# Kernel tuning notes

Hardware: AMD Instinct MI355X
Metric: run time of the kernel (lower is better)

## Reference

```python
import jax, jax.numpy as jnp
import numpy as np

D_MODEL = 1024
N_HEADS = 16
D_FF = 4096
EPS = 1e-6


def _linear_params(key, d_in, d_out):
    kw, kb = jax.random.split(key)
    bound = 1.0 / np.sqrt(d_in)
    W = jax.random.uniform(kw, (d_out, d_in), minval=-bound, maxval=bound, dtype=jnp.float32)
    b = jax.random.uniform(kb, (d_out,), minval=-bound, maxval=bound, dtype=jnp.float32)
    return W, b


def setup_inputs() -> dict:
    key = jax.random.key(0)
    keys = jax.random.split(key, 8)
    x = jax.random.normal(keys[0], (4, 2048, D_MODEL), dtype=jnp.float32)
    mask = jnp.ones((4, 1, 1, 2048), dtype=jnp.bool_)
    Wq, bq = _linear_params(keys[1], D_MODEL, D_MODEL)
    Wk, bk = _linear_params(keys[2], D_MODEL, D_MODEL)
    Wv, bv = _linear_params(keys[3], D_MODEL, D_MODEL)
    Wo, bo = _linear_params(keys[4], D_MODEL, D_MODEL)
    W1, b1 = _linear_params(keys[5], D_MODEL, D_FF)
    W2, b2 = _linear_params(keys[6], D_FF, D_MODEL)
    ln1_g = jnp.ones((D_MODEL,), jnp.float32); ln1_b = jnp.zeros((D_MODEL,), jnp.float32)
    ln2_g = jnp.ones((D_MODEL,), jnp.float32); ln2_b = jnp.zeros((D_MODEL,), jnp.float32)
    return {"x": x, "mask": mask,
            "Wq": Wq, "bq": bq, "Wk": Wk, "bk": bk, "Wv": Wv, "bv": bv,
            "Wo": Wo, "bo": bo, "W1": W1, "b1": b1, "W2": W2, "b2": b2,
            "ln1_g": ln1_g, "ln1_b": ln1_b, "ln2_g": ln2_g, "ln2_b": ln2_b}


def _layernorm(x, g, b):
    # torch LayerNorm here uses unbiased std and divides by (std + eps)
    mean = jnp.mean(x, axis=-1, keepdims=True)
    std = jnp.std(x, axis=-1, keepdims=True, ddof=1)
    return g * (x - mean) / (std + EPS) + b


def _gelu_tanh(x):
    c = np.sqrt(2.0 / np.pi).astype(np.float32)
    return 0.5 * x * (1.0 + jnp.tanh(c * (x + 0.044715 * x * x * x)))


def _mha(xn, mask, Wq, bq, Wk, bk, Wv, bv, Wo, bo):
    B, S, D = xn.shape
    d_k = D // N_HEADS
    def proj(W, b):
        y = jnp.einsum('bsd,ed->bse', xn, W) + b
        return y.reshape(B, S, N_HEADS, d_k).transpose(0, 2, 1, 3)  # [B,h,S,d_k]
    q, k, v = proj(Wq, bq), proj(Wk, bk), proj(Wv, bv)
    scores = jnp.einsum('bhqd,bhkd->bhqk', q, k) / np.float32(np.sqrt(d_k))
    scores = jnp.where(mask, scores, jnp.float32(-1e9))
    p = jax.nn.softmax(scores, axis=-1)
    o = jnp.einsum('bhqk,bhkd->bhqd', p, v)
    o = o.transpose(0, 2, 1, 3).reshape(B, S, D)
    return jnp.einsum('bsd,ed->bse', o, Wo) + bo


def reference(x, mask, Wq, bq, Wk, bk, Wv, bv, Wo, bo, W1, b1, W2, b2,
              ln1_g, ln1_b, ln2_g, ln2_b):
    xn = _layernorm(x, ln1_g, ln1_b)
    y = x + _mha(xn, mask, Wq, bq, Wk, bk, Wv, bv, Wo, bo)
    yn = _layernorm(y, ln2_g, ln2_b)
    h = _gelu_tanh(jnp.einsum('bsd,fd->bsf', yn, W1) + b1)
    z = y + (jnp.einsum('bsf,df->bsd', h, W2) + b2)
    return z
```

## Files before the change

### kernel.cpp

```cpp
#include <hip/hip_runtime.h>

typedef __bf16 bf16;
typedef __bf16 bfx4 __attribute__((ext_vector_type(4)));
typedef __bf16 bfx8 __attribute__((ext_vector_type(8)));
typedef float  fx4  __attribute__((ext_vector_type(4)));

#define NTOK 8192
#define DM   1024
#define DFF  4096
#define SEQ  2048
#define NH   16
#define DK   64

#define OFF_WQKV 0ull
#define OFF_WO   (OFF_WQKV + 3072ull*1024*2)
#define OFF_W1   (OFF_WO   + 1024ull*1024*2)
#define OFF_W2   (OFF_W1   + 4096ull*1024*2)
#define OFF_BQKV (OFF_W2   + 4096ull*1024*2)
#define OFF_XN   (OFF_BQKV + 3072ull*4)
#define OFF_QKV  (OFF_XN   + 8192ull*1024*2)
#define OFF_ATTN (OFF_QKV  + 8192ull*3072*2)
#define OFF_Y    (OFF_ATTN + 8192ull*1024*2)
#define OFF_VT   OFF_XN
#define OFF_H    OFF_XN
#define OFF_YN   OFF_ATTN

#define BARRIER() do { asm volatile("" ::: "memory"); \
                       __builtin_amdgcn_s_barrier();  \
                       asm volatile("" ::: "memory"); } while (0)

__device__ __forceinline__ void gload16(const void* g, void* l) {
  __builtin_amdgcn_global_load_lds(
      (__attribute__((address_space(1))) void*)(g),
      (__attribute__((address_space(3))) void*)(l), 16, 0, 0);
}

__device__ __forceinline__ float gelu_tanh(float x) {
  float u = 0.7978845608028654f * (x + 0.044715f * x * x * x);
  float t = 1.f - 2.f / (__expf(2.f * u) + 1.f);
  return 0.5f * x * (1.f + t);
}

__global__ __launch_bounds__(256) void castk(const float* __restrict__ s,
                                             bf16* __restrict__ d, int n) {
  int i = (blockIdx.x * 256 + threadIdx.x) * 4;
  if (i < n) {
    float4 v = *(const float4*)(s + i);
    bfx4 o;
    o[0] = (bf16)v.x; o[1] = (bf16)v.y; o[2] = (bf16)v.z; o[3] = (bf16)v.w;
    *(bfx4*)(d + i) = o;
  }
}

__global__ __launch_bounds__(256) void ln_kernel(const float* __restrict__ x,
                                                 const float* __restrict__ g,
                                                 const float* __restrict__ b,
                                                 bf16* __restrict__ out) {
  const int row = blockIdx.x;
  const int c = threadIdx.x * 4;
  const float4 v = *(const float4*)&x[(size_t)row * DM + c];
  float s1 = v.x + v.y + v.z + v.w;
  float s2 = v.x * v.x + v.y * v.y + v.z * v.z + v.w * v.w;
  #pragma unroll
  for (int o = 32; o; o >>= 1) { s1 += __shfl_xor(s1, o); s2 += __shfl_xor(s2, o); }
  __shared__ float red[8];
  const int wid = threadIdx.x >> 6;
  if ((threadIdx.x & 63) == 0) { red[wid] = s1; red[4 + wid] = s2; }
  __syncthreads();
  s1 = red[0] + red[1] + red[2] + red[3];
  s2 = red[4] + red[5] + red[6] + red[7];
  const float mean = s1 * (1.f / (float)DM);
  const float var = (s2 - (float)DM * mean * mean) * (1.f / (float)(DM - 1));
  const float inv = 1.f / (sqrtf(fmaxf(var, 0.f)) + 1e-6f);
  bfx4 o;
  o[0] = (bf16)(g[c + 0] * (v.x - mean) * inv + b[c + 0]);
  o[1] = (bf16)(g[c + 1] * (v.y - mean) * inv + b[c + 1]);
  o[2] = (bf16)(g[c + 2] * (v.z - mean) * inv + b[c + 2]);
  o[3] = (bf16)(g[c + 3] * (v.w - mean) * inv + b[c + 3]);
  *(bfx4*)&out[(size_t)row * DM + c] = o;
}

template <int NREP, int EPI>
__global__ __launch_bounds__(512, 2) void gemm256(const bf16* __restrict__ A,
                                                  const bf16* __restrict__ B,
                                                  const float* __restrict__ bias,
                                                  const float* __restrict__ resid,
                                                  void* __restrict__ outp,
                                                  int M, int N, int K) {
  extern __shared__ char lds[];
  constexpr int BHALF = NREP * 4096;
  const int tid = threadIdx.x;
  const int lane = tid & 63, w = tid >> 6;
  const int l15 = lane & 15, lhi = lane >> 4;
  const int wm = w >> 2, wn = w & 3;

  const int nwg = gridDim.x * gridDim.y;
  int bid = blockIdx.y * gridDim.x + blockIdx.x;
  bid = (bid & 7) * (nwg >> 3) + (bid >> 3);
  const int m0 = (bid % gridDim.x) * 256;
  const int n0 = (bid / gridDim.x) * (NREP * 64);

  const char* Ab = (const char*)A;
  const char* Bb = (const char*)B;
  const size_t str = (size_t)K * 2;

  const int r_s = tid >> 3;
  const int c2  = (tid & 7) * 16;
  const int csw = c2 ^ ((r_s & 7) << 4);

  auto stA = [&](int buf, int half, int kt) {
    const size_t kb = (size_t)kt * 128;
    #pragma unroll
    for (int s = 0; s < 2; ++s)
      gload16(Ab + (size_t)(m0 + half * 128 + s * 64 + r_s) * str + kb + csw,
              lds + (buf * 2 + half) * 16384 + s * 8192 + tid * 16);
  };
  auto stB = [&](int buf, int half, int kt) {
    const size_t kb = (size_t)kt * 128;
    #pragma unroll
    for (int s = 0; s < NREP / 2; ++s)
      gload16(Bb + (size_t)(n0 + half * (NREP * 32) + s * 64 + r_s) * str + kb + csw,
              lds + 65536 + (buf * 2 + half) * BHALF + s * 8192 + tid * 16);
  };

  fx4 acc[8][NREP] = {};
  bfx8 af[4][2];
  bfx8 bfv[NREP][2];
  const int asw = (l15 & 7) << 4;

  auto ldA = [&](int buf, int i0) {
    const char* base = lds + (buf * 2 + wm) * 16384;
    #pragma unroll
    for (int ii = 0; ii < 4; ++ii) {
      const int r = (i0 + ii) * 16 + l15;
      #pragma unroll
      for (int kk = 0; kk < 2; ++kk)
        af[ii][kk] = *(const bfx8*)(base + r * 128 + ((kk * 64 + lhi * 16) ^ asw));
    }
  };
  auto ldB = [&](int buf, int j0) {
    const char* base = lds + 65536 + (buf * 2 + (wn >> 1)) * BHALF;
    #pragma unroll
    for (int jj = 0; jj < NREP / 2; ++jj) {
      const int r = (wn & 1) * (NREP * 16) + (j0 + jj) * 16 + l15;
      #pragma unroll
      for (int kk = 0; kk < 2; ++kk)
        bfv[j0 + jj][kk] = *(const bfx8*)(base + r * 128 + ((kk * 64 + lhi * 16) ^ asw));
    }
  };
  auto mm = [&](int qm, int qn) {
    __builtin_amdgcn_s_setprio(1);
    #pragma unroll
    for (int ii = 0; ii < 4; ++ii)
      #pragma unroll
      for (int jj = 0; jj < NREP / 2; ++jj)
        #pragma unroll
        for (int kk = 0; kk < 2; ++kk)
          acc[qm * 4 + ii][qn * (NREP / 2) + jj] =
              __builtin_amdgcn_mfma_f32_16x16x32_bf16(
                  af[ii][kk], bfv[qn * (NREP / 2) + jj][kk],
                  acc[qm * 4 + ii][qn * (NREP / 2) + jj], 0, 0, 0);
    __builtin_amdgcn_s_setprio(0);
  };

  const int nK = K >> 6, niters = nK >> 1;

  stA(0, 0, 0); stA(0, 1, 0); stB(0, 0, 0); stB(0, 1, 0);
  stB(1, 0, 1); stB(1, 1, 1);
  asm volatile("s_waitcnt vmcnt(%0)" :: "i"(NREP) : "memory");
  BARRIER();

  #pragma unroll 1
  for (int it = 0; it < niters; ++it) {
    const int t1 = 2 * it + 1, t2 = 2 * it + 2, t3 = 2 * it + 3;
    const bool more = (it < niters - 1);
    ldA(0, 0); ldB(0, 0);
    stA(1, 0, t1);
    BARRIER(); mm(0, 0); BARRIER();
    ldB(0, NREP / 2);
    stA(1, 1, t1);
    BARRIER(); mm(0, 1); BARRIER();
    ldA(0, 4);
    if (more) stB(0, 0, t2);
    BARRIER(); mm(1, 0); BARRIER();
    if (more) {
      stB(0, 1, t2);
      asm volatile("s_waitcnt vmcnt(%0)" :: "i"(NREP) : "memory");
    } else {
      asm volatile("s_waitcnt vmcnt(0)" ::: "memory");
    }
    BARRIER(); mm(1, 1); BARRIER();
    ldA(1, 0); ldB(1, 0);
    if (more) stA(0, 0, t2);
    BARRIER(); mm(0, 0); BARRIER();
    ldB(1, NREP / 2);
    if (more) stA(0, 1, t2);
    BARRIER(); mm(0, 1); BARRIER();
    ldA(1, 4);
    if (more) stB(1, 0, t3);
    BARRIER(); mm(1, 0); BARRIER();
    if (more) {
      stB(1, 1, t3);
      asm volatile("s_waitcnt vmcnt(%0)" :: "i"(NREP) : "memory");
    }
    BARRIER(); mm(1, 1); BARRIER();
  }

  const int rb = m0 + wm * 128 + lhi * 4;
  const int cb = n0 + wn * 16 * NREP + l15;
  #pragma unroll
  for (int j = 0; j < NREP; ++j) {
    const int c = cb + j * 16;
    const float bv = bias[c];
    #pragma unroll
    for (int i = 0; i < 8; ++i) {
      #pragma unroll
      for (int e = 0; e < 4; ++e) {
        const size_t idx = (size_t)(rb + i * 16 + e) * N + c;
        float v = acc[i][j][e] + bv;
        if constexpr (EPI == 1) v = gelu_tanh(v);
        if constexpr (EPI == 2) {
          ((float*)outp)[idx] = v + resid[idx];
        } else {
          ((bf16*)outp)[idx] = (bf16)v;
        }
      }
    }
  }
}

__global__ __launch_bounds__(256) void vtrans(const bf16* __restrict__ QKV,
                                              bf16* __restrict__ VT) {
  __shared__ bf16 Ts[64][64];
  const int t = threadIdx.x;
  const int s0 = blockIdx.x * 64, bh = blockIdx.y;
  const int b = bh >> 4, h = bh & 15;
  const size_t tokb = (size_t)b * SEQ + s0;
  #pragma unroll
  for (int rr = 0; rr < 2; ++rr) {
    const int s = (t >> 3) + rr * 32;
    const int c0 = (t & 7) * 8;
    bfx8 v = *(const bfx8*)&QKV[(tokb + s) * 3072 + 2048 + h * 64 + c0];
    #pragma unroll
    for (int e = 0; e < 8; ++e) {
      const int d = c0 + e;
      Ts[d][(s + ((d >> 3) & 7) * 8) & 63] = v[e];
    }
  }
  __syncthreads();
  #pragma unroll
  for (int rr = 0; rr < 2; ++rr) {
    const int d = (t >> 3) + rr * 32;
    const int c0 = (t & 7) * 8;
    bfx8 v = *(const bfx8*)&Ts[d][(c0 + ((d >> 3) & 7) * 8) & 63];
    *(bfx8*)&VT[(size_t)(bh * 64 + d) * SEQ + s0 + c0] = v;
  }
}

__global__ __launch_bounds__(256) void attn_kernel(const bf16* __restrict__ QKV,
                                                   const bf16* __restrict__ VT,
                                                   bf16* __restrict__ O) {
  __shared__ bf16 lds[2][2][4096];
  const int tid = threadIdx.x;
  const int lane = tid & 63, w = tid >> 6;
  const int l15 = lane & 15, lhi = lane >> 4;
  int id = blockIdx.x;
  id = (id & 7) * 128 + (id >> 3);
  const int q0 = (id & 15) * 128;
  const int h = (id >> 4) & 15;
  const int b = id >> 8;
  const size_t tokbase = (size_t)b * SEQ;
  const char* Kb  = (const char*)QKV;
  const char* Vtb = (const char*)(VT + (size_t)((b * NH + h) * 64) * SEQ);

  fx4 acc[2][4] = {};
  float mrun[2] = {-3e38f, -3e38f};
  float lrun[2] = {0.f, 0.f};

  auto STAGE = [&](int t, int buf) {
    const int kv0 = t * 64;
    #pragma unroll
    for (int seg = 0; seg < 2; ++seg) {
      const int lin = (seg * 4 + w) * 1024 + lane * 16;
      const int row = lin >> 7, cbyte = lin & 127;
      const int cs = cbyte ^ ((row & 7) << 4);
      gload16(Kb + ((tokbase + kv0 + row) * 3072 + 1024 + h * 64) * 2 + cs,
              (char*)&lds[buf][0][0] + lin);
      gload16(Vtb + ((size_t)row * SEQ + kv0) * 2 + cs,
              (char*)&lds[buf][1][0] + lin);
    }
  };

  STAGE(0, 0);

  bfx8 qf[2][2];
  #pragma unroll
  for (int m = 0; m < 2; ++m)
    #pragma unroll
    for (int kk = 0; kk < 2; ++kk) {
      bfx8 raw = *(const bfx8*)&QKV[(tokbase + q0 + w * 32 + m * 16 + l15) * 3072
                                    + h * DK + kk * 32 + lhi * 8];
      bfx8 sc;
      #pragma unroll
      for (int e = 0; e < 8; ++e) sc[e] = (bf16)((float)raw[e] * 0.18033688011112042f);
      qf[m][kk] = sc;
    }

  const int NT = SEQ / 64;
  for (int t = 0; t < NT; ++t) {
    const int buf = t & 1;
    if (t + 1 < NT) {
      STAGE(t + 1, buf ^ 1);
      asm volatile("s_waitcnt vmcnt(4)" ::: "memory");
    } else {
      asm volatile("s_waitcnt vmcnt(0)" ::: "memory");
    }
    __builtin_amdgcn_s_barrier();

    const char* Kl = (const char*)&lds[buf][0][0];
    const char* Vl = (const char*)&lds[buf][1][0];

    fx4 s[2][4] = {};
    #pragma unroll
    for (int kk = 0; kk < 2; ++kk) {
      bfx8 kf[4];
      #pragma unroll
      for (int n = 0; n < 4; ++n) {
        const int row = n * 16 + l15;
        kf[n] = *(const bfx8*)(Kl + row * 128 + ((kk * 64 + lhi * 16) ^ ((row & 7) << 4)));
      }
      #pragma unroll
      for (int m = 0; m < 2; ++m)
        #pragma unroll
        for (int n = 0; n < 4; ++n)
          s[m][n] = __builtin_amdgcn_mfma_f32_16x16x32_bf16(kf[n], qf[m][kk], s[m][n], 0, 0, 0);
    }

    uint32_t pu[2][4][2];
    #pragma unroll
    for (int m = 0; m < 2; ++m) {
      float rm = s[m][0][0];
      #pragma unroll
      for (int n = 0; n < 4; ++n)
        #pragma unroll
        for (int e = 0; e < 4; ++e) rm = fmaxf(rm, s[m][n][e]);
      rm = fmaxf(rm, __shfl_xor(rm, 16));
      rm = fmaxf(rm, __shfl_xor(rm, 32));
      const float mnew = fmaxf(mrun[m], rm);
      const float alpha = exp2f(mrun[m] - mnew);
      mrun[m] = mnew;
      float rs = 0.f;
      #pragma unroll
      for (int n = 0; n < 4; ++n)
        #pragma unroll
        for (int e = 0; e < 4; ++e) {
          const float p = exp2f(s[m][n][e] - mnew);
          s[m][n][e] = p;
          rs += p;
        }
      rs += __shfl_xor(rs, 16);
      rs += __shfl_xor(rs, 32);
      lrun[m] = lrun[m] * alpha + rs;
      #pragma unroll
      for (int dn = 0; dn < 4; ++dn)
        #pragma unroll
        for (int e = 0; e < 4; ++e) acc[m][dn][e] *= alpha;
      #pragma unroll
      for (int n = 0; n < 4; ++n)
        #pragma unroll
        for (int p2 = 0; p2 < 2; ++p2) {
          union { bf16 h2[2]; uint32_t u; } cv;
          cv.h2[0] = (bf16)s[m][n][2 * p2];
          cv.h2[1] = (bf16)s[m][n][2 * p2 + 1];
          pu[m][n][p2] = cv.u;
        }
    }

    #pragma unroll
    for (int kk = 0; kk < 2; ++kk) {
      bfx8 pB[2];
      #pragma unroll
      for (int m = 0; m < 2; ++m) {
        union { uint32_t u[4]; bfx8 v; } cb2;
        cb2.u[0] = pu[m][2 * kk][0];
        cb2.u[1] = pu[m][2 * kk][1];
        cb2.u[2] = pu[m][2 * kk + 1][0];
        cb2.u[3] = pu[m][2 * kk + 1][1];
        pB[m] = cb2.v;
      }
      #pragma unroll
      for (int dn = 0; dn < 4; ++dn) {
        const int row = dn * 16 + l15;
        const int sw = (row & 7) << 4;
        union { bfx4 q2[2]; bfx8 v; } vv;
        vv.q2[0] = *(const bfx4*)(Vl + row * 128 + ((kk * 64 + lhi * 8) ^ sw));
        vv.q2[1] = *(const bfx4*)(Vl + row * 128 + ((kk * 64 + 32 + lhi * 8) ^ sw));
        #pragma unroll
        for (int m = 0; m < 2; ++m)
          acc[m][dn] = __builtin_amdgcn_mfma_f32_16x16x32_bf16(vv.v, pB[m], acc[m][dn], 0, 0, 0);
      }
    }

    asm volatile("s_waitcnt lgkmcnt(0)" ::: "memory");
    __builtin_amdgcn_s_barrier();
  }

  __syncthreads();
  bf16* Ep = &lds[0][0][0] + w * 2048;
  const float rinv0 = __builtin_amdgcn_rcpf(lrun[0]);
  const float rinv1 = __builtin_amdgcn_rcpf(lrun[1]);
  #pragma unroll
  for (int m = 0; m < 2; ++m) {
    const int qr = m * 16 + l15;
    const int sw = (qr & 7) << 4;
    const float ri = m ? rinv1 : rinv0;
    #pragma unroll
    for (int dn = 0; dn < 4; ++dn)
      #pragma unroll
      for (int e = 0; e < 4; ++e) {
        const int d = dn * 16 + lhi * 4 + e;
        *(bf16*)((char*)Ep + qr * 128 + ((2 * d) ^ sw)) = (bf16)(acc[m][dn][e] * ri);
      }
  }
  __syncthreads();
  #pragma unroll
  for (int j = 0; j < 4; ++j) {
    const int qr = lane >> 1;
    const int cbyte = (lane & 1) * 64 + j * 16;
    bfx8 v = *(const bfx8*)((char*)Ep + qr * 128 + (cbyte ^ ((qr & 7) << 4)));
    *(bfx8*)&O[(tokbase + q0 + w * 32 + qr) * (size_t)DM + h * DK + (lane & 1) * 32 + j * 8] = v;
  }
}

extern "C" void kernel_launch(void* const* d_in, const int* in_sizes, int n_in,
                              void* d_out, int out_size, void* d_ws, size_t ws_size,
                              hipStream_t stream) {
  const float* x  = (const float*)d_in[0];
  const float* Wq = (const float*)d_in[2];
  const float* bq = (const float*)d_in[3];
  const float* Wk = (const float*)d_in[4];
  const float* bk = (const float*)d_in[5];
  const float* Wv = (const float*)d_in[6];
  const float* bv = (const float*)d_in[7];
  const float* Wo = (const float*)d_in[8];
  const float* bo = (const float*)d_in[9];
  const float* W1 = (const float*)d_in[10];
  const float* b1 = (const float*)d_in[11];
  const float* W2 = (const float*)d_in[12];
  const float* b2 = (const float*)d_in[13];
  const float* g1 = (const float*)d_in[14];
  const float* be1 = (const float*)d_in[15];
  const float* g2 = (const float*)d_in[16];
  const float* be2 = (const float*)d_in[17];

  char* ws = (char*)d_ws;
  bf16* WQKVb = (bf16*)(ws + OFF_WQKV);
  bf16* WOb   = (bf16*)(ws + OFF_WO);
  bf16* W1b   = (bf16*)(ws + OFF_W1);
  bf16* W2b   = (bf16*)(ws + OFF_W2);
  float* BQKV = (float*)(ws + OFF_BQKV);
  bf16* XN    = (bf16*)(ws + OFF_XN);
  bf16* QKVb  = (bf16*)(ws + OFF_QKV);
  bf16* ATTNb = (bf16*)(ws + OFF_ATTN);
  float* Yb   = (float*)(ws + OFF_Y);
  bf16* VTb   = (bf16*)(ws + OFF_VT);
  bf16* Hb    = (bf16*)(ws + OFF_H);
  bf16* YNb   = (bf16*)(ws + OFF_YN);

  hipFuncSetAttribute((const void*)&gemm256<4, 0>,
                      hipFuncAttributeMaxDynamicSharedMemorySize, 131072);
  hipFuncSetAttribute((const void*)&gemm256<4, 1>,
                      hipFuncAttributeMaxDynamicSharedMemorySize, 131072);
  hipFuncSetAttribute((const void*)&gemm256<2, 2>,
                      hipFuncAttributeMaxDynamicSharedMemorySize, 98304);

  castk<<<1024, 256, 0, stream>>>(Wq, WQKVb,               1024 * 1024);
  castk<<<1024, 256, 0, stream>>>(Wk, WQKVb + 1024 * 1024, 1024 * 1024);
  castk<<<1024, 256, 0, stream>>>(Wv, WQKVb + 2048 * 1024, 1024 * 1024);
  castk<<<1024, 256, 0, stream>>>(Wo, WOb, 1024 * 1024);
  castk<<<4096, 256, 0, stream>>>(W1, W1b, 4096 * 1024);
  castk<<<4096, 256, 0, stream>>>(W2, W2b, 4096 * 1024);
  hipMemcpyAsync(BQKV,        bq, 4096, hipMemcpyDeviceToDevice, stream);
  hipMemcpyAsync(BQKV + 1024, bk, 4096, hipMemcpyDeviceToDevice, stream);
  hipMemcpyAsync(BQKV + 2048, bv, 4096, hipMemcpyDeviceToDevice, stream);

  ln_kernel<<<NTOK, 256, 0, stream>>>(x, g1, be1, XN);
  gemm256<4, 0><<<dim3(32, 12), 512, 131072, stream>>>(XN, WQKVb, BQKV, nullptr,
                                                       QKVb, NTOK, 3072, 1024);
  vtrans<<<dim3(SEQ / 64, 64), 256, 0, stream>>>(QKVb, VTb);
  attn_kernel<<<1024, 256, 0, stream>>>(QKVb, VTb, ATTNb);
  gemm256<2, 2><<<dim3(32, 8), 512, 98304, stream>>>(ATTNb, WOb, bo, x, Yb,
                                                     NTOK, 1024, 1024);
  ln_kernel<<<NTOK, 256, 0, stream>>>(Yb, g2, be2, YNb);
  gemm256<4, 1><<<dim3(32, 16), 512, 131072, stream>>>(YNb, W1b, b1, nullptr,
                                                       Hb, NTOK, 4096, 1024);
  gemm256<2, 2><<<dim3(32, 8), 512, 98304, stream>>>(Hb, W2b, b2, Yb,
                                                     (float*)d_out, NTOK, 1024, 4096);
}
```

Measured before the change: 489.1 us.

## Merge weight-cast launches and streamline the attention inner loop

Replaces six weight-cast kernels and three bias memcpys with one combined cast kernel and a small bias-copy kernel, cutting launch overhead. The attention kernel uses pointer-increment staging, raises occupancy via launch bounds, and unrolls the KV loop by two. It skips the running-max rescale unless the new max exceeds the old by more than a threshold (lazy rescaling), computes the softmax row sum with an MFMA against a ones vector, and raises wave priority around MFMA blocks. The lazy rescale lets exponents grow up to 2^8 before renormalising, which is safe in fp32 but changes rounding slightly.

```diff
diff --git a/kernel.cpp b/kernel.cpp
--- a/kernel.cpp
+++ b/kernel.cpp
@@ -41,15 +41,36 @@
   return 0.5f * x * (1.f + t);
 }
 
-__global__ __launch_bounds__(256) void castk(const float* __restrict__ s,
-                                             bf16* __restrict__ d, int n) {
-  int i = (blockIdx.x * 256 + threadIdx.x) * 4;
-  if (i < n) {
-    float4 v = *(const float4*)(s + i);
-    bfx4 o;
-    o[0] = (bf16)v.x; o[1] = (bf16)v.y; o[2] = (bf16)v.z; o[3] = (bf16)v.w;
-    *(bfx4*)(d + i) = o;
-  }
+__global__ __launch_bounds__(256) void cast_all(const float* __restrict__ Wq,
+                                                const float* __restrict__ Wk,
+                                                const float* __restrict__ Wv,
+                                                const float* __restrict__ Wo,
+                                                const float* __restrict__ W1,
+                                                const float* __restrict__ W2,
+                                                bf16* __restrict__ dst) {
+  const int bid = blockIdx.x;
+  const int g = bid >> 9;
+  const int j = ((bid & 511) << 11) + threadIdx.x * 8;
+  const float* s;
+  if (g == 0) s = Wq;
+  else if (g == 1) s = Wk;
+  else if (g == 2) s = Wv;
+  else if (g == 3) s = Wo;
+  else if (g < 8) s = W1 + (size_t)(g - 4) * 1048576;
+  else s = W2 + (size_t)(g - 8) * 1048576;
+  const float4 a = *(const float4*)(s + j);
+  const float4 c = *(const float4*)(s + j + 4);
+  bfx8 o;
+  o[0] = (bf16)a.x; o[1] = (bf16)a.y; o[2] = (bf16)a.z; o[3] = (bf16)a.w;
+  o[4] = (bf16)c.x; o[5] = (bf16)c.y; o[6] = (bf16)c.z; o[7] = (bf16)c.w;
+  *(bfx8*)(dst + (size_t)g * 1048576 + j) = o;
+}
+
+__global__ void biask(const float* __restrict__ bq, const float* __restrict__ bk,
+                      const float* __restrict__ bv, float* __restrict__ o) {
+  const int i = blockIdx.x * 1024 + threadIdx.x;
+  const float* s = blockIdx.x == 0 ? bq : (blockIdx.x == 1 ? bk : bv);
+  o[i] = s[threadIdx.x];
 }
 
 __global__ __launch_bounds__(256) void ln_kernel(const float* __restrict__ x,
@@ -257,9 +278,9 @@
   }
 }
 
-__global__ __launch_bounds__(256) void attn_kernel(const bf16* __restrict__ QKV,
-                                                   const bf16* __restrict__ VT,
-                                                   bf16* __restrict__ O) {
+__global__ __launch_bounds__(256, 4) void attn_kernel(const bf16* __restrict__ QKV,
+                                                      const bf16* __restrict__ VT,
+                                                      bf16* __restrict__ O) {
   __shared__ bf16 lds[2][2][4096];
   const int tid = threadIdx.x;
   const int lane = tid & 63, w = tid >> 6;
@@ -270,28 +291,32 @@
   const int h = (id >> 4) & 15;
   const int b = id >> 8;
   const size_t tokbase = (size_t)b * SEQ;
-  const char* Kb  = (const char*)QKV;
-  const char* Vtb = (const char*)(VT + (size_t)((b * NH + h) * 64) * SEQ);
-
-  fx4 acc[2][4] = {};
-  float mrun[2] = {-3e38f, -3e38f};
-  float lrun[2] = {0.f, 0.f};
-
-  auto STAGE = [&](int t, int buf) {
-    const int kv0 = t * 64;
-    #pragma unroll
-    for (int seg = 0; seg < 2; ++seg) {
-      const int lin = (seg * 4 + w) * 1024 + lane * 16;
-      const int row = lin >> 7, cbyte = lin & 127;
-      const int cs = cbyte ^ ((row & 7) << 4);
-      gload16(Kb + ((tokbase + kv0 + row) * 3072 + 1024 + h * 64) * 2 + cs,
-              (char*)&lds[buf][0][0] + lin);
-      gload16(Vtb + ((size_t)row * SEQ + kv0) * 2 + cs,
-              (char*)&lds[buf][1][0] + lin);
-    }
+
+  const int lin0 = w * 1024 + lane * 16;
+  const int lin1 = lin0 + 4096;
+  const int row0 = lin0 >> 7, row1 = lin1 >> 7;
+  const int cs0 = (lin0 & 127) ^ ((row0 & 7) << 4);
+  const int cs1 = (lin1 & 127) ^ ((row1 & 7) << 4);
+  const char* kp0 = (const char*)QKV + ((tokbase + row0) * 3072 + 1024 + h * 64) * 2 + cs0;
+  const char* kp1 = (const char*)QKV + ((tokbase + row1) * 3072 + 1024 + h * 64) * 2 + cs1;
+  const char* vbase = (const char*)(VT + (size_t)((b * NH + h) * 64) * SEQ);
+  const char* vp0 = vbase + (size_t)row0 * (SEQ * 2) + cs0;
+  const char* vp1 = vbase + (size_t)row1 * (SEQ * 2) + cs1;
+  char* const ldsb = (char*)&lds[0][0][0];
+  int dofs = 0;
+  const long KADV = 64l * 3072 * 2;
+  const long VADV = 64l * 2;
+
+  auto stage = [&]() {
+    gload16(kp0, ldsb + dofs + lin0);
+    gload16(kp1, ldsb + dofs + lin1);
+    gload16(vp0, ldsb + dofs + 8192 + lin0);
+    gload16(vp1, ldsb + dofs + 8192 + lin1);
+    kp0 += KADV; kp1 += KADV; vp0 += VADV; vp1 += VADV;
+    dofs ^= 16384;
   };
 
-  STAGE(0, 0);
+  stage();
 
   bfx8 qf[2][2];
   #pragma unroll
@@ -306,19 +331,26 @@
       qf[m][kk] = sc;
     }
 
+  fx4 acc[2][4] = {};
+  fx4 lsum[2] = {};
+  float mrun[2] = {-3e38f, -3e38f};
+  bfx8 ones;
+  #pragma unroll
+  for (int e = 0; e < 8; ++e) ones[e] = (bf16)1.0f;
+
   const int NT = SEQ / 64;
+  #pragma unroll 2
   for (int t = 0; t < NT; ++t) {
-    const int buf = t & 1;
     if (t + 1 < NT) {
-      STAGE(t + 1, buf ^ 1);
+      stage();
       asm volatile("s_waitcnt vmcnt(4)" ::: "memory");
     } else {
       asm volatile("s_waitcnt vmcnt(0)" ::: "memory");
     }
     __builtin_amdgcn_s_barrier();
 
-    const char* Kl = (const char*)&lds[buf][0][0];
-    const char* Vl = (const char*)&lds[buf][1][0];
+    const char* Kl = ldsb + ((t & 1) << 14);
+    const char* Vl = Kl + 8192;
 
     fx4 s[2][4] = {};
     #pragma unroll
@@ -329,51 +361,47 @@
         const int row = n * 16 + l15;
         kf[n] = *(const bfx8*)(Kl + row * 128 + ((kk * 64 + lhi * 16) ^ ((row & 7) << 4)));
       }
+      __builtin_amdgcn_s_setprio(1);
       #pragma unroll
       for (int m = 0; m < 2; ++m)
         #pragma unroll
         for (int n = 0; n < 4; ++n)
           s[m][n] = __builtin_amdgcn_mfma_f32_16x16x32_bf16(kf[n], qf[m][kk], s[m][n], 0, 0, 0);
+      __builtin_amdgcn_s_setprio(0);
     }
 
     uint32_t pu[2][4][2];
     #pragma unroll
     for (int m = 0; m < 2; ++m) {
-      float rm = s[m][0][0];
-      #pragma unroll
-      for (int n = 0; n < 4; ++n)
-        #pragma unroll
-        for (int e = 0; e < 4; ++e) rm = fmaxf(rm, s[m][n][e]);
+      const float r0 = fmaxf(fmaxf(s[m][0][0], s[m][0][1]), fmaxf(s[m][0][2], s[m][0][3]));
+      const float r1 = fmaxf(fmaxf(s[m][1][0], s[m][1][1]), fmaxf(s[m][1][2], s[m][1][3]));
+      const float r2 = fmaxf(fmaxf(s[m][2][0], s[m][2][1]), fmaxf(s[m][2][2], s[m][2][3]));
+      const float r3 = fmaxf(fmaxf(s[m][3][0], s[m][3][1]), fmaxf(s[m][3][2], s[m][3][3]));
+      float rm = fmaxf(fmaxf(r0, r1), fmaxf(r2, r3));
       rm = fmaxf(rm, __shfl_xor(rm, 16));
       rm = fmaxf(rm, __shfl_xor(rm, 32));
-      const float mnew = fmaxf(mrun[m], rm);
-      const float alpha = exp2f(mrun[m] - mnew);
-      mrun[m] = mnew;
-      float rs = 0.f;
-      #pragma unroll
-      for (int n = 0; n < 4; ++n)
+      if (!__all(rm <= mrun[m] + 8.f)) {
+        const float mnew = fmaxf(mrun[m], rm);
+        const float alpha = exp2f(mrun[m] - mnew);
+        mrun[m] = mnew;
         #pragma unroll
-        for (int e = 0; e < 4; ++e) {
-          const float p = exp2f(s[m][n][e] - mnew);
-          s[m][n][e] = p;
-          rs += p;
-        }
-      rs += __shfl_xor(rs, 16);
-      rs += __shfl_xor(rs, 32);
-      lrun[m] = lrun[m] * alpha + rs;
-      #pragma unroll
-      for (int dn = 0; dn < 4; ++dn)
-        #pragma unroll
-        for (int e = 0; e < 4; ++e) acc[m][dn][e] *= alpha;
-      #pragma unroll
-      for (int n = 0; n < 4; ++n)
-        #pragma unroll
-        for (int p2 = 0; p2 < 2; ++p2) {
-          union { bf16 h2[2]; uint32_t u; } cv;
-          cv.h2[0] = (bf16)s[m][n][2 * p2];
-          cv.h2[1] = (bf16)s[m][n][2 * p2 + 1];
-          pu[m][n][p2] = cv.u;
-        }
+        for (int dn = 0; dn < 4; ++dn)
+          #pragma unroll
+          for (int e = 0; e < 4; ++e) acc[m][dn][e] *= alpha;
+        lsum[m][0] *= alpha;
+      }
+      const float mm_ = mrun[m];
+      #pragma unroll
+      for (int n = 0; n < 4; ++n) {
+        const float p0 = exp2f(s[m][n][0] - mm_);
+        const float p1 = exp2f(s[m][n][1] - mm_);
+        const float p2 = exp2f(s[m][n][2] - mm_);
+        const float p3 = exp2f(s[m][n][3] - mm_);
+        union { bf16 h2[2]; uint32_t u; } c0, c1;
+        c0.h2[0] = (bf16)p0; c0.h2[1] = (bf16)p1;
+        c1.h2[0] = (bf16)p2; c1.h2[1] = (bf16)p3;
+        pu[m][n][0] = c0.u; pu[m][n][1] = c1.u;
+      }
     }
 
     #pragma unroll
@@ -388,6 +416,11 @@
         cb2.u[3] = pu[m][2 * kk + 1][1];
         pB[m] = cb2.v;
       }
+      __builtin_amdgcn_s_setprio(1);
+      #pragma unroll
+      for (int m = 0; m < 2; ++m)
+        lsum[m] = __builtin_amdgcn_mfma_f32_16x16x32_bf16(ones, pB[m], lsum[m], 0, 0, 0);
+      __builtin_amdgcn_s_setprio(0);
       #pragma unroll
       for (int dn = 0; dn < 4; ++dn) {
         const int row = dn * 16 + l15;
@@ -395,9 +428,11 @@
         union { bfx4 q2[2]; bfx8 v; } vv;
         vv.q2[0] = *(const bfx4*)(Vl + row * 128 + ((kk * 64 + lhi * 8) ^ sw));
         vv.q2[1] = *(const bfx4*)(Vl + row * 128 + ((kk * 64 + 32 + lhi * 8) ^ sw));
+        __builtin_amdgcn_s_setprio(1);
         #pragma unroll
         for (int m = 0; m < 2; ++m)
           acc[m][dn] = __builtin_amdgcn_mfma_f32_16x16x32_bf16(vv.v, pB[m], acc[m][dn], 0, 0, 0);
+        __builtin_amdgcn_s_setprio(0);
       }
     }
 
@@ -407,8 +442,8 @@
 
   __syncthreads();
   bf16* Ep = &lds[0][0][0] + w * 2048;
-  const float rinv0 = __builtin_amdgcn_rcpf(lrun[0]);
-  const float rinv1 = __builtin_amdgcn_rcpf(lrun[1]);
+  const float rinv0 = __builtin_amdgcn_rcpf(lsum[0][0]);
+  const float rinv1 = __builtin_amdgcn_rcpf(lsum[1][0]);
   #pragma unroll
   for (int m = 0; m < 2; ++m) {
     const int qr = m * 16 + l15;
@@ -474,15 +509,8 @@
   hipFuncSetAttribute((const void*)&gemm256<2, 2>,
                       hipFuncAttributeMaxDynamicSharedMemorySize, 98304);
 
-  castk<<<1024, 256, 0, stream>>>(Wq, WQKVb,               1024 * 1024);
-  castk<<<1024, 256, 0, stream>>>(Wk, WQKVb + 1024 * 1024, 1024 * 1024);
-  castk<<<1024, 256, 0, stream>>>(Wv, WQKVb + 2048 * 1024, 1024 * 1024);
-  castk<<<1024, 256, 0, stream>>>(Wo, WOb, 1024 * 1024);
-  castk<<<4096, 256, 0, stream>>>(W1, W1b, 4096 * 1024);
-  castk<<<4096, 256, 0, stream>>>(W2, W2b, 4096 * 1024);
-  hipMemcpyAsync(BQKV,        bq, 4096, hipMemcpyDeviceToDevice, stream);
-  hipMemcpyAsync(BQKV + 1024, bk, 4096, hipMemcpyDeviceToDevice, stream);
-  hipMemcpyAsync(BQKV + 2048, bv, 4096, hipMemcpyDeviceToDevice, stream);
+  cast_all<<<6144, 256, 0, stream>>>(Wq, Wk, Wv, Wo, W1, W2, WQKVb);
+  biask<<<3, 1024, 0, stream>>>(bq, bk, bv, BQKV);
 
   ln_kernel<<<NTOK, 256, 0, stream>>>(x, g1, be1, XN);
   gemm256<4, 0><<<dim3(32, 12), 512, 131072, stream>>>(XN, WQKVb, BQKV, nullptr,
```

New measurement: 478.6 us. 2.1% less time.
